# Performance work log

Measured on AMD Instinct MI355X. Metric: run time of the kernel, lower is better.

## Reference

```python
import jax, jax.numpy as jnp
import numpy as np

N = 100000      # nodes
E = 3200000     # edges (avg degree 32)
D = 128         # in_channels
H = 128         # hidden_channels
L = 4           # num_layers
G = 1000        # graphs in batch
C = 10          # out_channels
BN_EPS = 1e-5


def _init(key, shape, fan_in):
    return jax.random.normal(key, shape, jnp.float32) * jnp.float32(1.0 / np.sqrt(fan_in))


def setup_inputs() -> dict:
    key = jax.random.key(0)
    ks = jax.random.split(key, 12)
    x = jax.random.normal(ks[0], (N, D), jnp.float32)
    edge_index = jax.random.randint(ks[1], (2, E), 0, N)
    batch = jnp.sort(jax.random.randint(ks[2], (N,), 0, G))
    # stacked per-layer GINConv MLP params (in==hidden so all layers share shapes)
    W1 = _init(ks[3], (L, D, 2 * H), D)
    b1 = jnp.zeros((L, 2 * H), jnp.float32)
    g1 = jnp.ones((L, 2 * H), jnp.float32)
    bt1 = jnp.zeros((L, 2 * H), jnp.float32)
    W2 = _init(ks[4], (L, 2 * H, H), 2 * H)
    b2 = jnp.zeros((L, H), jnp.float32)
    g2 = jnp.ones((L, H), jnp.float32)
    bt2 = jnp.zeros((L, H), jnp.float32)
    eps = jnp.zeros((L,), jnp.float32)  # train_eps=True, init 0
    # final graph-level MLP
    Wm1 = _init(ks[5], (H, H), H)
    bm1 = jnp.zeros((H,), jnp.float32)
    gm = jnp.ones((H,), jnp.float32)
    btm = jnp.zeros((H,), jnp.float32)
    Wm2 = _init(ks[6], (H, C), H)
    bm2 = jnp.zeros((C,), jnp.float32)
    return dict(x=x, edge_index=edge_index, batch=batch, eps=eps,
                W1=W1, b1=b1, g1=g1, bt1=bt1, W2=W2, b2=b2, g2=g2, bt2=bt2,
                Wm1=Wm1, bm1=bm1, gm=gm, btm=btm, Wm2=Wm2, bm2=bm2)


def batchnorm(z, g, b):
    # training-mode BN: batch statistics, biased variance (torch semantics)
    m = jnp.mean(z, axis=0)
    v = jnp.mean(jnp.square(z - m), axis=0)
    return (z - m) * (g * jax.lax.rsqrt(v + BN_EPS)) + b


def reference(x, edge_index, batch, eps, W1, b1, g1, bt1, W2, b2, g2, bt2,
              Wm1, bm1, gm, btm, Wm2, bm2):
    src, dst = edge_index[0], edge_index[1]
    h = x
    for l in range(L):
        # GINConv: (1+eps)*x_i + sum_{j in N(i)} x_j, then MLP
        agg = jax.ops.segment_sum(h[src], dst, num_segments=N)  # [N, d]
        z = (1.0 + eps[l]) * h + agg
        z = jax.nn.relu(batchnorm(z @ W1[l] + b1[l], g1[l], bt1[l]))
        h = z @ W2[l] + b2[l]
        # outer per-layer BatchNorm + relu
        h = jax.nn.relu(batchnorm(h, g2[l], bt2[l]))
    # global_add_pool over graphs
    ge = jax.ops.segment_sum(h, batch, num_segments=G)  # [G, H]
    o = jax.nn.relu(batchnorm(ge @ Wm1 + bm1, gm, btm))  # dropout = identity (eval)
    return o @ Wm2 + bm2  # [G, C]
```

## Files before the change

### kernel.cpp

```cpp
#include <hip/hip_runtime.h>

#define N_NODES 100000
#define N_EDGES 3200000
#define NGRAPH  1000
#define NOUT    10
#define BN_EPS  1e-5f
#define CAP     96

#define SUM1 0
#define SQ1  256
#define S1   512
#define SH1  768
#define SUM2 1024
#define SQ2  1152
#define S2   1280
#define SH2  1408
#define SUMG 1536
#define SQG  1664
#define SG   1792
#define SHG  1920

typedef short v8s __attribute__((ext_vector_type(8)));
typedef float v4f __attribute__((ext_vector_type(4)));

__device__ __forceinline__ unsigned short f2bf(float x) {
    unsigned u = __float_as_uint(x);
    u += 0x7FFFu + ((u >> 16) & 1u);
    return (unsigned short)(u >> 16);
}
__device__ __forceinline__ float bf2f(unsigned short h) {
    return __uint_as_float(((unsigned)h) << 16);
}


__global__ void k_zero_i(int* p, int n) {
    int i = blockIdx.x * 256 + threadIdx.x;
    if (i < n) p[i] = 0;
}

__global__ void k_fillb(const int* __restrict__ ei, int* __restrict__ cnt,
                        int* __restrict__ csr) {
    const int lo = blockIdx.x * 12500;
    const int base = blockIdx.y * 2048 + threadIdx.x;
#pragma unroll
    for (int i = 0; i < 8; ++i) {
        int e = base + i * 256;
        if (e < N_EDGES) {
            int d = ei[N_EDGES + e];
            if ((unsigned)(d - lo) < 12500u) {
                int slot = atomicAdd(&cnt[d], 1);
                if (slot < CAP) csr[d * CAP + slot] = ei[e];
            }
        }
    }
}


__global__ void k_cvt0(const float* __restrict__ x, unsigned short* __restrict__ hb) {
    int i = blockIdx.x * 256 + threadIdx.x;
    float4 v = ((const float4*)x)[i];
    ushort4 o;
    o.x = f2bf(v.x); o.y = f2bf(v.y); o.z = f2bf(v.z); o.w = f2bf(v.w);
    ((ushort4*)hb)[i] = o;
}


__global__ void k_wsplit(const float* __restrict__ W1l, const float* __restrict__ W2l,
                         unsigned short* __restrict__ w1h, unsigned short* __restrict__ w1lo,
                         unsigned short* __restrict__ w2h, unsigned short* __restrict__ w2lo) {
    int idx = blockIdx.x * 256 + threadIdx.x;
    if (idx < 32768) {
        float v = W1l[idx];
        int k = idx >> 8, n = idx & 255;
        unsigned short h = f2bf(v);
        unsigned short l = f2bf(v - bf2f(h));
        int o = n * 128 + k;
        w1h[o] = h; w1lo[o] = l;
    } else {
        int i2 = idx - 32768;
        float v = W2l[i2];
        int k = i2 >> 7, n = i2 & 127;
        unsigned short h = f2bf(v);
        unsigned short l = f2bf(v - bf2f(h));
        int o = n * 256 + k;
        w2h[o] = h; w2lo[o] = l;
    }
}


template <bool BN>
__launch_bounds__(256)
__global__ void k_agg(const unsigned short* __restrict__ hb, unsigned short* __restrict__ zh,
                      unsigned short* __restrict__ zl, const int* __restrict__ cnt,
                      const int* __restrict__ csr, const float* __restrict__ eps, int l,
                      float* __restrict__ stats, const float* __restrict__ s,
                      const float* __restrict__ sh) {
    if (blockIdx.x == 0) {
        int t = threadIdx.x;
        stats[SUM1 + t] = 0.f;
        stats[SQ1 + t] = 0.f;
        if (t < 128) { stats[SUM2 + t] = 0.f; stats[SQ2 + t] = 0.f; }
    }
    int gtid = blockIdx.x * 256 + threadIdx.x;
    int node = gtid >> 6;
    int lane = gtid & 63;
    float2 sv = make_float2(1.f, 1.f), shv = make_float2(0.f, 0.f);
    if (BN) { sv = ((const float2*)s)[lane]; shv = ((const float2*)sh)[lane]; }
    float epv = 1.f + eps[l];
    const unsigned* h2 = (const unsigned*)hb;

    auto conv = [&](unsigned u) -> float2 {
        float a = bf2f((unsigned short)(u & 0xffffu));
        float b = bf2f((unsigned short)(u >> 16));
        if (BN) {
            a = fmaxf(fmaf(a, sv.x, shv.x), 0.f);
            b = fmaxf(fmaf(b, sv.y, shv.y), 0.f);
        }
        return make_float2(a, b);
    };

    float2 self = conv(h2[(size_t)node * 64 + lane]);
    float accx = epv * self.x, accy = epv * self.y;
    int d = min(cnt[node], CAP);
    const int* row = csr + node * CAP;
    int t = 0;
    for (; t + 1 < d; t += 2) {
        int j0 = row[t], j1 = row[t + 1];
        float2 v0 = conv(h2[(size_t)j0 * 64 + lane]);
        float2 v1 = conv(h2[(size_t)j1 * 64 + lane]);
        accx += v0.x + v1.x;
        accy += v0.y + v1.y;
    }
    if (t < d) {
        float2 v = conv(h2[(size_t)row[t] * 64 + lane]);
        accx += v.x;
        accy += v.y;
    }
    unsigned short hx = f2bf(accx), hy = f2bf(accy);
    unsigned short lx = f2bf(accx - bf2f(hx)), ly = f2bf(accy - bf2f(hy));
    ((unsigned*)zh)[(size_t)node * 64 + lane] = (unsigned)hx | ((unsigned)hy << 16);
    ((unsigned*)zl)[(size_t)node * 64 + lane] = (unsigned)lx | ((unsigned)ly << 16);
}


template <int K, int NC>
__launch_bounds__(256, 2)
__global__ void k_mgemm1(const unsigned short* __restrict__ Azh,
                         const unsigned short* __restrict__ Azl,
                         const unsigned short* __restrict__ Bhi,
                         const unsigned short* __restrict__ Blo,
                         const float* __restrict__ bias, float* __restrict__ Cm, int M,
                         float* __restrict__ osum, float* __restrict__ osq) {
    __shared__ unsigned short Ash[128 * 72];
    __shared__ unsigned short Asl[128 * 72];
    __shared__ unsigned short Bsh[128 * 72];
    __shared__ unsigned short Bsl[128 * 72];
    const int tid = threadIdx.x;
    const int lane = tid & 63;
    const int wid = tid >> 6;
    const int wm = wid >> 1, wn = wid & 1;
    const int lr = lane & 15;
    const int q = lane >> 4;
    const int r0 = blockIdx.x * 128;
    const int c0 = blockIdx.y * 128;

    v4f acc[16];
#pragma unroll
    for (int i = 0; i < 16; ++i) acc[i] = (v4f){0.f, 0.f, 0.f, 0.f};

    for (int kc = 0; kc < K; kc += 64) {
#pragma unroll
        for (int it = 0; it < 4; ++it) {
            int li = it * 256 + tid;
            int row = li >> 3, s8 = li & 7;
            int r = r0 + row;
            float4 vh = make_float4(0.f, 0.f, 0.f, 0.f);
            float4 vl = vh;
            if (r < M) {
                size_t go = (size_t)r * K + kc + s8 * 8;
                vh = *(const float4*)(Azh + go);
                vl = *(const float4*)(Azl + go);
            }
            int off = row * 72 + s8 * 8;
            *(float4*)&Ash[off] = vh;
            *(float4*)&Asl[off] = vl;
        }
#pragma unroll
        for (int it = 0; it < 4; ++it) {
            int li = it * 256 + tid;
            int n = li >> 3, s8 = li & 7;
            int off = n * 72 + s8 * 8;
            size_t go = (size_t)(c0 + n) * K + kc + s8 * 8;
            *(float4*)&Bsh[off] = *(const float4*)(Bhi + go);
            *(float4*)&Bsl[off] = *(const float4*)(Blo + go);
        }
        __syncthreads();
#pragma unroll
        for (int kk = 0; kk < 2; ++kk) {
            v8s ah[4], al[4], bh[4], bl[4];
#pragma unroll
            for (int t = 0; t < 4; ++t) {
                int aoff = (wm * 64 + t * 16 + lr) * 72 + kk * 32 + q * 8;
                ah[t] = *(const v8s*)&Ash[aoff];
                al[t] = *(const v8s*)&Asl[aoff];
                int boff = (wn * 64 + t * 16 + lr) * 72 + kk * 32 + q * 8;
                bh[t] = *(const v8s*)&Bsh[boff];
                bl[t] = *(const v8s*)&Bsl[boff];
            }
#pragma unroll
            for (int mt = 0; mt < 4; ++mt)
#pragma unroll
                for (int nt = 0; nt < 4; ++nt)
                    acc[mt * 4 + nt] = __builtin_amdgcn_mfma_f32_16x16x32_bf16(
                        ah[mt], bh[nt], acc[mt * 4 + nt], 0, 0, 0);
#pragma unroll
            for (int mt = 0; mt < 4; ++mt)
#pragma unroll
                for (int nt = 0; nt < 4; ++nt)
                    acc[mt * 4 + nt] = __builtin_amdgcn_mfma_f32_16x16x32_bf16(
                        ah[mt], bl[nt], acc[mt * 4 + nt], 0, 0, 0);
#pragma unroll
            for (int mt = 0; mt < 4; ++mt)
#pragma unroll
                for (int nt = 0; nt < 4; ++nt)
                    acc[mt * 4 + nt] = __builtin_amdgcn_mfma_f32_16x16x32_bf16(
                        al[mt], bh[nt], acc[mt * 4 + nt], 0, 0, 0);
        }
        __syncthreads();
    }

    float bias_v[4];
#pragma unroll
    for (int nt = 0; nt < 4; ++nt) bias_v[nt] = bias[c0 + wn * 64 + nt * 16 + lr];
    float ps[4] = {0.f, 0.f, 0.f, 0.f}, pq[4] = {0.f, 0.f, 0.f, 0.f};
#pragma unroll
    for (int mt = 0; mt < 4; ++mt) {
        int rb = r0 + wm * 64 + mt * 16 + q * 4;
#pragma unroll
        for (int r = 0; r < 4; ++r) {
            int row = rb + r;
            if (row < M) {
#pragma unroll
                for (int nt = 0; nt < 4; ++nt) {
                    float o = acc[mt * 4 + nt][r] + bias_v[nt];
                    Cm[(size_t)row * NC + c0 + wn * 64 + nt * 16 + lr] = o;
                    ps[nt] += o;
                    pq[nt] += o * o;
                }
            }
        }
    }
#pragma unroll
    for (int nt = 0; nt < 4; ++nt) {
        ps[nt] += __shfl_down(ps[nt], 16);
        ps[nt] += __shfl_down(ps[nt], 32);
        pq[nt] += __shfl_down(pq[nt], 16);
        pq[nt] += __shfl_down(pq[nt], 32);
    }
    if (lane < 16) {
#pragma unroll
        for (int nt = 0; nt < 4; ++nt) {
            int col = c0 + wn * 64 + nt * 16 + lane;
            atomicAdd(&osum[col], ps[nt]);
            atomicAdd(&osq[col], pq[nt]);
        }
    }
}


template <int K, int NC>
__launch_bounds__(256, 2)
__global__ void k_mgemm2(const float* __restrict__ A, const unsigned short* __restrict__ Bhi,
                         const unsigned short* __restrict__ Blo, const float* __restrict__ bias,
                         unsigned short* __restrict__ Cb, int M,
                         const float* __restrict__ ain_s, const float* __restrict__ ain_sh,
                         float* __restrict__ osum, float* __restrict__ osq) {
    __shared__ unsigned short Ash[128 * 72];
    __shared__ unsigned short Asl[128 * 72];
    __shared__ unsigned short Bsh[128 * 72];
    __shared__ unsigned short Bsl[128 * 72];
    const int tid = threadIdx.x;
    const int lane = tid & 63;
    const int wid = tid >> 6;
    const int wm = wid >> 1, wn = wid & 1;
    const int lr = lane & 15;
    const int q = lane >> 4;
    const int r0 = blockIdx.x * 128;
    const int c0 = blockIdx.y * 128;

    v4f acc[16];
#pragma unroll
    for (int i = 0; i < 16; ++i) acc[i] = (v4f){0.f, 0.f, 0.f, 0.f};

    for (int kc = 0; kc < K; kc += 64) {
#pragma unroll
        for (int it = 0; it < 8; ++it) {
            int li = it * 256 + tid;
            int row = li >> 4, s4 = li & 15;
            int r = r0 + row;
            float4 v = make_float4(0.f, 0.f, 0.f, 0.f);
            if (r < M) {
                v = *(const float4*)(A + (size_t)r * K + kc + s4 * 4);
                float4 s = *(const float4*)(ain_s + kc + s4 * 4);
                float4 h = *(const float4*)(ain_sh + kc + s4 * 4);
                v.x = fmaxf(fmaf(v.x, s.x, h.x), 0.f);
                v.y = fmaxf(fmaf(v.y, s.y, h.y), 0.f);
                v.z = fmaxf(fmaf(v.z, s.z, h.z), 0.f);
                v.w = fmaxf(fmaf(v.w, s.w, h.w), 0.f);
            }
            unsigned short h0 = f2bf(v.x), h1 = f2bf(v.y), h2 = f2bf(v.z), h3 = f2bf(v.w);
            unsigned short l0 = f2bf(v.x - bf2f(h0)), l1 = f2bf(v.y - bf2f(h1));
            unsigned short l2 = f2bf(v.z - bf2f(h2)), l3 = f2bf(v.w - bf2f(h3));
            int off = row * 72 + s4 * 4;
            *(short4*)&Ash[off] = make_short4((short)h0, (short)h1, (short)h2, (short)h3);
            *(short4*)&Asl[off] = make_short4((short)l0, (short)l1, (short)l2, (short)l3);
        }
#pragma unroll
        for (int it = 0; it < 4; ++it) {
            int li = it * 256 + tid;
            int n = li >> 3, s8 = li & 7;
            int off = n * 72 + s8 * 8;
            size_t go = (size_t)(c0 + n) * K + kc + s8 * 8;
            *(float4*)&Bsh[off] = *(const float4*)(Bhi + go);
            *(float4*)&Bsl[off] = *(const float4*)(Blo + go);
        }
        __syncthreads();
#pragma unroll
        for (int kk = 0; kk < 2; ++kk) {
            v8s ah[4], al[4], bh[4], bl[4];
#pragma unroll
            for (int t = 0; t < 4; ++t) {
                int aoff = (wm * 64 + t * 16 + lr) * 72 + kk * 32 + q * 8;
                ah[t] = *(const v8s*)&Ash[aoff];
                al[t] = *(const v8s*)&Asl[aoff];
                int boff = (wn * 64 + t * 16 + lr) * 72 + kk * 32 + q * 8;
                bh[t] = *(const v8s*)&Bsh[boff];
                bl[t] = *(const v8s*)&Bsl[boff];
            }
#pragma unroll
            for (int mt = 0; mt < 4; ++mt)
#pragma unroll
                for (int nt = 0; nt < 4; ++nt)
                    acc[mt * 4 + nt] = __builtin_amdgcn_mfma_f32_16x16x32_bf16(
                        ah[mt], bh[nt], acc[mt * 4 + nt], 0, 0, 0);
#pragma unroll
            for (int mt = 0; mt < 4; ++mt)
#pragma unroll
                for (int nt = 0; nt < 4; ++nt)
                    acc[mt * 4 + nt] = __builtin_amdgcn_mfma_f32_16x16x32_bf16(
                        ah[mt], bl[nt], acc[mt * 4 + nt], 0, 0, 0);
#pragma unroll
            for (int mt = 0; mt < 4; ++mt)
#pragma unroll
                for (int nt = 0; nt < 4; ++nt)
                    acc[mt * 4 + nt] = __builtin_amdgcn_mfma_f32_16x16x32_bf16(
                        al[mt], bh[nt], acc[mt * 4 + nt], 0, 0, 0);
        }
        __syncthreads();
    }

    float bias_v[4];
#pragma unroll
    for (int nt = 0; nt < 4; ++nt) bias_v[nt] = bias[c0 + wn * 64 + nt * 16 + lr];
    float ps[4] = {0.f, 0.f, 0.f, 0.f}, pq[4] = {0.f, 0.f, 0.f, 0.f};
#pragma unroll
    for (int mt = 0; mt < 4; ++mt) {
        int rb = r0 + wm * 64 + mt * 16 + q * 4;
#pragma unroll
        for (int r = 0; r < 4; ++r) {
            int row = rb + r;
            if (row < M) {
#pragma unroll
                for (int nt = 0; nt < 4; ++nt) {
                    float o = acc[mt * 4 + nt][r] + bias_v[nt];
                    Cb[(size_t)row * NC + c0 + wn * 64 + nt * 16 + lr] = f2bf(o);
                    ps[nt] += o;
                    pq[nt] += o * o;
                }
            }
        }
    }
#pragma unroll
    for (int nt = 0; nt < 4; ++nt) {
        ps[nt] += __shfl_down(ps[nt], 16);
        ps[nt] += __shfl_down(ps[nt], 32);
        pq[nt] += __shfl_down(pq[nt], 16);
        pq[nt] += __shfl_down(pq[nt], 32);
    }
    if (lane < 16) {
#pragma unroll
        for (int nt = 0; nt < 4; ++nt) {
            int col = c0 + wn * 64 + nt * 16 + lane;
            atomicAdd(&osum[col], ps[nt]);
            atomicAdd(&osq[col], pq[nt]);
        }
    }
}


template <int K, int NC, bool AIN, bool STATS>
__launch_bounds__(256)
__global__ void k_gemm(const float* __restrict__ A, const float* __restrict__ Bg,
                       const float* __restrict__ bias, float* __restrict__ Cm, int M,
                       const float* __restrict__ ain_s, const float* __restrict__ ain_sh,
                       float* __restrict__ osum, float* __restrict__ osq) {
    __shared__ __align__(16) float As[64][68];
    __shared__ __align__(16) float Bs[64][68];
    const int tid = threadIdx.x;
    const int tx = tid & 15, ty = tid >> 4;
    const int r0 = blockIdx.x * 64;
    const int c0 = blockIdx.y * 64;
    float acc[4][4] = {};

    for (int kc = 0; kc < K; kc += 64) {
#pragma unroll
        for (int it = 0; it < 4; ++it) {
            int li = it * 256 + tid;
            int row = li >> 4, f4 = li & 15;
            int r = r0 + row;
            float4 v = make_float4(0.f, 0.f, 0.f, 0.f);
            if (r < M) v = *(const float4*)(A + (size_t)r * K + kc + f4 * 4);
            As[f4 * 4 + 0][row] = v.x;
            As[f4 * 4 + 1][row] = v.y;
            As[f4 * 4 + 2][row] = v.z;
            As[f4 * 4 + 3][row] = v.w;
        }
#pragma unroll
        for (int it = 0; it < 4; ++it) {
            int li = it * 256 + tid;
            int krow = li >> 4, f4 = li & 15;
            float4 v = *(const float4*)(Bg + (size_t)(kc + krow) * NC + c0 + f4 * 4);
            *(float4*)&Bs[krow][f4 * 4] = v;
        }
        __syncthreads();
#pragma unroll
        for (int k = 0; k < 64; ++k) {
            float4 a = *(const float4*)&As[k][ty * 4];
            float4 b = *(const float4*)&Bs[k][tx * 4];
            float av[4] = {a.x, a.y, a.z, a.w};
            float bv[4] = {b.x, b.y, b.z, b.w};
#pragma unroll
            for (int i = 0; i < 4; ++i)
#pragma unroll
                for (int j = 0; j < 4; ++j) acc[i][j] = fmaf(av[i], bv[j], acc[i][j]);
        }
        __syncthreads();
    }

    const int c = c0 + tx * 4;
    float4 bb = *(const float4*)(bias + c);
    float bvv[4] = {bb.x, bb.y, bb.z, bb.w};
    float ps[4] = {0.f, 0.f, 0.f, 0.f};
    float pq[4] = {0.f, 0.f, 0.f, 0.f};
#pragma unroll
    for (int i = 0; i < 4; ++i) {
        int r = r0 + ty * 4 + i;
        if (r < M) {
            float o[4];
#pragma unroll
            for (int j = 0; j < 4; ++j) {
                o[j] = acc[i][j] + bvv[j];
                if (STATS) { ps[j] += o[j]; pq[j] += o[j] * o[j]; }
            }
            float4 ov = make_float4(o[0], o[1], o[2], o[3]);
            *(float4*)(Cm + (size_t)r * NC + c) = ov;
        }
    }
    if (STATS) {
        float* rs = &As[0][0];
        float* rq = &Bs[0][0];
        *(float4*)&rs[ty * 68 + tx * 4] = make_float4(ps[0], ps[1], ps[2], ps[3]);
        *(float4*)&rq[ty * 68 + tx * 4] = make_float4(pq[0], pq[1], pq[2], pq[3]);
        __syncthreads();
        if (tid < 16) {
#pragma unroll
            for (int j = 0; j < 4; ++j) {
                float s = 0.f, q = 0.f;
                for (int t = 0; t < 16; ++t) {
                    s += rs[t * 68 + tid * 4 + j];
                    q += rq[t * 68 + tid * 4 + j];
                }
                atomicAdd(&osum[c0 + tid * 4 + j], s);
                atomicAdd(&osq[c0 + tid * 4 + j], q);
            }
        }
    }
}


__global__ void k_bnstats(const float* __restrict__ sum, const float* __restrict__ sq,
                          const float* __restrict__ g, const float* __restrict__ bt,
                          float* __restrict__ s, float* __restrict__ sh, int n, float invM) {
    int i = threadIdx.x;
    if (i < n) {
        float m = sum[i] * invM;
        float v = sq[i] * invM - m * m;
        float sc = g[i] * rsqrtf(v + BN_EPS);
        s[i] = sc;
        sh[i] = bt[i] - m * sc;
    }
}


__global__ void k_zero2_f(float* p1, int n1, float* p2, int n2) {
    int i = blockIdx.x * 256 + threadIdx.x;
    if (i < n1) p1[i] = 0.f;
    else if (i - n1 < n2) p2[i - n1] = 0.f;
}

__global__ void k_pool(const unsigned short* __restrict__ hb, const int* __restrict__ batch,
                       float* __restrict__ ge, const float* __restrict__ s,
                       const float* __restrict__ sh) {
    int t = blockIdx.x * 256 + threadIdx.x;
    int node = t >> 6, lane = t & 63;
    int g = batch[node];
    unsigned u = ((const unsigned*)hb)[(size_t)node * 64 + lane];
    float2 sv = ((const float2*)s)[lane];
    float2 shv = ((const float2*)sh)[lane];
    float a = fmaxf(fmaf(bf2f((unsigned short)(u & 0xffffu)), sv.x, shv.x), 0.f);
    float b = fmaxf(fmaf(bf2f((unsigned short)(u >> 16)), sv.y, shv.y), 0.f);
    float* p = ge + (size_t)g * 128 + lane * 2;
    atomicAdd(p, a);
    atomicAdd(p + 1, b);
}


__global__ void k_final(const float* __restrict__ gmid, const float* __restrict__ sg,
                        const float* __restrict__ shg, const float* __restrict__ Wm2,
                        const float* __restrict__ bm2, float* __restrict__ out) {
    int idx = blockIdx.x * 256 + threadIdx.x;
    if (idx >= NGRAPH * NOUT) return;
    int g = idx / NOUT, c = idx % NOUT;
    const float* row = gmid + (size_t)g * 128;
    float acc = bm2[c];
#pragma unroll 8
    for (int k = 0; k < 128; ++k) {
        float y = fmaxf(fmaf(row[k], sg[k], shg[k]), 0.f);
        acc = fmaf(y, Wm2[k * NOUT + c], acc);
    }
    out[idx] = acc;
}


extern "C" void kernel_launch(void* const* d_in, const int* in_sizes, int n_in,
                              void* d_out, int out_size, void* d_ws, size_t ws_size,
                              hipStream_t stream) {
    const float* x   = (const float*)d_in[0];
    const int*   ei  = (const int*)d_in[1];
    const int* batch = (const int*)d_in[2];
    const float* eps = (const float*)d_in[3];
    const float* W1  = (const float*)d_in[4];
    const float* b1  = (const float*)d_in[5];
    const float* g1  = (const float*)d_in[6];
    const float* bt1 = (const float*)d_in[7];
    const float* W2  = (const float*)d_in[8];
    const float* b2  = (const float*)d_in[9];
    const float* g2  = (const float*)d_in[10];
    const float* bt2 = (const float*)d_in[11];
    const float* Wm1 = (const float*)d_in[12];
    const float* bm1 = (const float*)d_in[13];
    const float* gm  = (const float*)d_in[14];
    const float* btm = (const float*)d_in[15];
    const float* Wm2 = (const float*)d_in[16];
    const float* bm2 = (const float*)d_in[17];
    float* out = (float*)d_out;

    float* W = (float*)d_ws;
    float* bufC  = W;
    float* stats = W + 25600000;
    float* ge    = W + 25602048;
    float* gmid  = W + 25730048;
    int* ib      = (int*)(W + 25858048);
    int* cnt = ib;
    int* csr = ib + 100000;
    unsigned short* wt = (unsigned short*)(ib + 9700000);
    unsigned short* w1h = wt;
    unsigned short* w1l = wt + 32768;
    unsigned short* w2h = wt + 65536;
    unsigned short* w2l = wt + 98304;
    unsigned short* hb = wt + 131072;
    unsigned short* zh = hb + 12800000;
    unsigned short* zl = zh + 12800000;

    k_zero_i<<<391, 256, 0, stream>>>(cnt, N_NODES);
    k_fillb<<<dim3(8, 1563), 256, 0, stream>>>(ei, cnt, csr);
    k_cvt0<<<12500, 256, 0, stream>>>(x, hb);

    for (int l = 0; l < 4; ++l) {
        k_wsplit<<<256, 256, 0, stream>>>(W1 + l * 32768, W2 + l * 32768,
                                          w1h, w1l, w2h, w2l);
        if (l == 0)
            k_agg<false><<<25000, 256, 0, stream>>>(hb, zh, zl, cnt, csr, eps, l, stats,
                                                    nullptr, nullptr);
        else
            k_agg<true><<<25000, 256, 0, stream>>>(hb, zh, zl, cnt, csr, eps, l, stats,
                                                   stats + S2, stats + SH2);
        k_mgemm1<128, 256><<<dim3(782, 2), 256, 0, stream>>>(
            zh, zl, w1h, w1l, b1 + l * 256, bufC, N_NODES, stats + SUM1, stats + SQ1);
        k_bnstats<<<1, 256, 0, stream>>>(stats + SUM1, stats + SQ1, g1 + l * 256,
                                         bt1 + l * 256, stats + S1, stats + SH1, 256,
                                         1.f / N_NODES);
        k_mgemm2<256, 128><<<dim3(782, 1), 256, 0, stream>>>(
            bufC, w2h, w2l, b2 + l * 128, hb, N_NODES,
            stats + S1, stats + SH1, stats + SUM2, stats + SQ2);
        k_bnstats<<<1, 128, 0, stream>>>(stats + SUM2, stats + SQ2, g2 + l * 128,
                                         bt2 + l * 128, stats + S2, stats + SH2, 128,
                                         1.f / N_NODES);
    }

    k_zero2_f<<<502, 256, 0, stream>>>(ge, 128000, stats + SUMG, 256);
    k_pool<<<25000, 256, 0, stream>>>(hb, batch, ge, stats + S2, stats + SH2);
    k_gemm<128, 128, false, true><<<dim3(16, 2), 256, 0, stream>>>(
        ge, Wm1, bm1, gmid, NGRAPH, nullptr, nullptr, stats + SUMG, stats + SQG);
    k_bnstats<<<1, 128, 0, stream>>>(stats + SUMG, stats + SQG, gm, btm,
                                     stats + SG, stats + SHG, 128, 1.f / NGRAPH);
    k_final<<<40, 256, 0, stream>>>(gmid, stats + SG, stats + SHG, Wm2, bm2, out);
}
```

Before: 1.782 ms.

## Precompute BN+ReLU activations once and widen aggregation gathers to 16-byte loads

Adds a k_bnapply pass that applies the previous layer's BN scale/shift and ReLU to every node once, writing a bf16 copy. Aggregation can then gather already-normalised rows instead of redoing the affine and ReLU for each of the ~32 edges per node. The gather kernel now assigns 16 lanes per node with uint4 loads (8 bf16 channels per lane) and reads neighbour indices as int4, so each load instruction moves more data. Pooling is also reworked so each thread sums 8 consecutive nodes and flushes atomics only when the graph id changes, cutting atomic traffic. The cost is an extra full read and write of the activation buffer per layer and a larger workspace.

```diff
diff --git a/kernel.cpp b/kernel.cpp
--- a/kernel.cpp
+++ b/kernel.cpp
@@ -62,6 +62,31 @@
     ushort4 o;
     o.x = f2bf(v.x); o.y = f2bf(v.y); o.z = f2bf(v.z); o.w = f2bf(v.w);
     ((ushort4*)hb)[i] = o;
+}
+
+
+__global__ void k_bnapply(const unsigned short* __restrict__ hb,
+                          unsigned short* __restrict__ yb,
+                          const float* __restrict__ s, const float* __restrict__ sh) {
+    int i = blockIdx.x * 256 + threadIdx.x;
+    int c16 = i & 15;
+    uint4 u = ((const uint4*)hb)[i];
+    float4 sA = ((const float4*)s)[c16 * 2], sB = ((const float4*)s)[c16 * 2 + 1];
+    float4 hA = ((const float4*)sh)[c16 * 2], hB = ((const float4*)sh)[c16 * 2 + 1];
+    float y0 = fmaxf(fmaf(__uint_as_float(u.x << 16),        sA.x, hA.x), 0.f);
+    float y1 = fmaxf(fmaf(__uint_as_float(u.x & 0xffff0000u), sA.y, hA.y), 0.f);
+    float y2 = fmaxf(fmaf(__uint_as_float(u.y << 16),        sA.z, hA.z), 0.f);
+    float y3 = fmaxf(fmaf(__uint_as_float(u.y & 0xffff0000u), sA.w, hA.w), 0.f);
+    float y4 = fmaxf(fmaf(__uint_as_float(u.z << 16),        sB.x, hB.x), 0.f);
+    float y5 = fmaxf(fmaf(__uint_as_float(u.z & 0xffff0000u), sB.y, hB.y), 0.f);
+    float y6 = fmaxf(fmaf(__uint_as_float(u.w << 16),        sB.z, hB.z), 0.f);
+    float y7 = fmaxf(fmaf(__uint_as_float(u.w & 0xffff0000u), sB.w, hB.w), 0.f);
+    uint4 o;
+    o.x = (unsigned)f2bf(y0) | ((unsigned)f2bf(y1) << 16);
+    o.y = (unsigned)f2bf(y2) | ((unsigned)f2bf(y3) << 16);
+    o.z = (unsigned)f2bf(y4) | ((unsigned)f2bf(y5) << 16);
+    o.w = (unsigned)f2bf(y6) | ((unsigned)f2bf(y7) << 16);
+    ((uint4*)yb)[i] = o;
 }
 
 
@@ -88,58 +113,103 @@
 }
 
 
-template <bool BN>
 __launch_bounds__(256)
-__global__ void k_agg(const unsigned short* __restrict__ hb, unsigned short* __restrict__ zh,
+__global__ void k_agg(const unsigned short* __restrict__ yb, unsigned short* __restrict__ zh,
                       unsigned short* __restrict__ zl, const int* __restrict__ cnt,
                       const int* __restrict__ csr, const float* __restrict__ eps, int l,
-                      float* __restrict__ stats, const float* __restrict__ s,
-                      const float* __restrict__ sh) {
+                      float* __restrict__ stats) {
     if (blockIdx.x == 0) {
         int t = threadIdx.x;
         stats[SUM1 + t] = 0.f;
         stats[SQ1 + t] = 0.f;
         if (t < 128) { stats[SUM2 + t] = 0.f; stats[SQ2 + t] = 0.f; }
     }
-    int gtid = blockIdx.x * 256 + threadIdx.x;
-    int node = gtid >> 6;
-    int lane = gtid & 63;
-    float2 sv = make_float2(1.f, 1.f), shv = make_float2(0.f, 0.f);
-    if (BN) { sv = ((const float2*)s)[lane]; shv = ((const float2*)sh)[lane]; }
+    const int tid = threadIdx.x;
+    const int wid = tid >> 6, lane = tid & 63;
+    const int q = lane >> 4, sl = lane & 15;
+    const int node = blockIdx.x * 16 + wid * 4 + q;
+    const uint4* y4 = (const uint4*)yb;
+    const size_t selfo = (size_t)node * 16 + sl;
+
     float epv = 1.f + eps[l];
-    const unsigned* h2 = (const unsigned*)hb;
-
-    auto conv = [&](unsigned u) -> float2 {
-        float a = bf2f((unsigned short)(u & 0xffffu));
-        float b = bf2f((unsigned short)(u >> 16));
-        if (BN) {
-            a = fmaxf(fmaf(a, sv.x, shv.x), 0.f);
-            b = fmaxf(fmaf(b, sv.y, shv.y), 0.f);
-        }
-        return make_float2(a, b);
-    };
-
-    float2 self = conv(h2[(size_t)node * 64 + lane]);
-    float accx = epv * self.x, accy = epv * self.y;
+    uint4 su = y4[selfo];
+    float acc[8];
+    acc[0] = epv * __uint_as_float(su.x << 16);
+    acc[1] = epv * __uint_as_float(su.x & 0xffff0000u);
+    acc[2] = epv * __uint_as_float(su.y << 16);
+    acc[3] = epv * __uint_as_float(su.y & 0xffff0000u);
+    acc[4] = epv * __uint_as_float(su.z << 16);
+    acc[5] = epv * __uint_as_float(su.z & 0xffff0000u);
+    acc[6] = epv * __uint_as_float(su.w << 16);
+    acc[7] = epv * __uint_as_float(su.w & 0xffff0000u);
+
     int d = min(cnt[node], CAP);
     const int* row = csr + node * CAP;
     int t = 0;
-    for (; t + 1 < d; t += 2) {
-        int j0 = row[t], j1 = row[t + 1];
-        float2 v0 = conv(h2[(size_t)j0 * 64 + lane]);
-        float2 v1 = conv(h2[(size_t)j1 * 64 + lane]);
-        accx += v0.x + v1.x;
-        accy += v0.y + v1.y;
-    }
-    if (t < d) {
-        float2 v = conv(h2[(size_t)row[t] * 64 + lane]);
-        accx += v.x;
-        accy += v.y;
-    }
-    unsigned short hx = f2bf(accx), hy = f2bf(accy);
-    unsigned short lx = f2bf(accx - bf2f(hx)), ly = f2bf(accy - bf2f(hy));
-    ((unsigned*)zh)[(size_t)node * 64 + lane] = (unsigned)hx | ((unsigned)hy << 16);
-    ((unsigned*)zl)[(size_t)node * 64 + lane] = (unsigned)lx | ((unsigned)ly << 16);
+    for (; t + 3 < d; t += 4) {
+        int4 jv = *(const int4*)(row + t);
+        uint4 v0 = y4[(size_t)jv.x * 16 + sl];
+        uint4 v1 = y4[(size_t)jv.y * 16 + sl];
+        uint4 v2 = y4[(size_t)jv.z * 16 + sl];
+        uint4 v3 = y4[(size_t)jv.w * 16 + sl];
+        acc[0] += __uint_as_float(v0.x << 16);
+        acc[1] += __uint_as_float(v0.x & 0xffff0000u);
+        acc[2] += __uint_as_float(v0.y << 16);
+        acc[3] += __uint_as_float(v0.y & 0xffff0000u);
+        acc[4] += __uint_as_float(v0.z << 16);
+        acc[5] += __uint_as_float(v0.z & 0xffff0000u);
+        acc[6] += __uint_as_float(v0.w << 16);
+        acc[7] += __uint_as_float(v0.w & 0xffff0000u);
+        acc[0] += __uint_as_float(v1.x << 16);
+        acc[1] += __uint_as_float(v1.x & 0xffff0000u);
+        acc[2] += __uint_as_float(v1.y << 16);
+        acc[3] += __uint_as_float(v1.y & 0xffff0000u);
+        acc[4] += __uint_as_float(v1.z << 16);
+        acc[5] += __uint_as_float(v1.z & 0xffff0000u);
+        acc[6] += __uint_as_float(v1.w << 16);
+        acc[7] += __uint_as_float(v1.w & 0xffff0000u);
+        acc[0] += __uint_as_float(v2.x << 16);
+        acc[1] += __uint_as_float(v2.x & 0xffff0000u);
+        acc[2] += __uint_as_float(v2.y << 16);
+        acc[3] += __uint_as_float(v2.y & 0xffff0000u);
+        acc[4] += __uint_as_float(v2.z << 16);
+        acc[5] += __uint_as_float(v2.z & 0xffff0000u);
+        acc[6] += __uint_as_float(v2.w << 16);
+        acc[7] += __uint_as_float(v2.w & 0xffff0000u);
+        acc[0] += __uint_as_float(v3.x << 16);
+        acc[1] += __uint_as_float(v3.x & 0xffff0000u);
+        acc[2] += __uint_as_float(v3.y << 16);
+        acc[3] += __uint_as_float(v3.y & 0xffff0000u);
+        acc[4] += __uint_as_float(v3.z << 16);
+        acc[5] += __uint_as_float(v3.z & 0xffff0000u);
+        acc[6] += __uint_as_float(v3.w << 16);
+        acc[7] += __uint_as_float(v3.w & 0xffff0000u);
+    }
+    for (; t < d; ++t) {
+        uint4 v = y4[(size_t)row[t] * 16 + sl];
+        acc[0] += __uint_as_float(v.x << 16);
+        acc[1] += __uint_as_float(v.x & 0xffff0000u);
+        acc[2] += __uint_as_float(v.y << 16);
+        acc[3] += __uint_as_float(v.y & 0xffff0000u);
+        acc[4] += __uint_as_float(v.z << 16);
+        acc[5] += __uint_as_float(v.z & 0xffff0000u);
+        acc[6] += __uint_as_float(v.w << 16);
+        acc[7] += __uint_as_float(v.w & 0xffff0000u);
+    }
+
+    unsigned oh[4], ol[4];
+#pragma unroll
+    for (int w = 0; w < 4; ++w) {
+        float a = acc[2 * w], b = acc[2 * w + 1];
+        unsigned short ha = f2bf(a), hb_ = f2bf(b);
+        unsigned short la = f2bf(a - bf2f(ha)), lb = f2bf(b - bf2f(hb_));
+        oh[w] = (unsigned)ha | ((unsigned)hb_ << 16);
+        ol[w] = (unsigned)la | ((unsigned)lb << 16);
+    }
+    uint4 vh; vh.x = oh[0]; vh.y = oh[1]; vh.z = oh[2]; vh.w = oh[3];
+    uint4 vl; vl.x = ol[0]; vl.y = ol[1]; vl.z = ol[2]; vl.w = ol[3];
+    ((uint4*)zh)[selfo] = vh;
+    ((uint4*)zl)[selfo] = vl;
 }
 
 
@@ -512,16 +582,30 @@
                        float* __restrict__ ge, const float* __restrict__ s,
                        const float* __restrict__ sh) {
     int t = blockIdx.x * 256 + threadIdx.x;
-    int node = t >> 6, lane = t & 63;
-    int g = batch[node];
-    unsigned u = ((const unsigned*)hb)[(size_t)node * 64 + lane];
-    float2 sv = ((const float2*)s)[lane];
-    float2 shv = ((const float2*)sh)[lane];
-    float a = fmaxf(fmaf(bf2f((unsigned short)(u & 0xffffu)), sv.x, shv.x), 0.f);
-    float b = fmaxf(fmaf(bf2f((unsigned short)(u >> 16)), sv.y, shv.y), 0.f);
-    float* p = ge + (size_t)g * 128 + lane * 2;
-    atomicAdd(p, a);
-    atomicAdd(p + 1, b);
+    int c = t & 63;
+    int n0 = (t >> 6) * 8;
+    float2 sv = ((const float2*)s)[c];
+    float2 shv = ((const float2*)sh)[c];
+    const unsigned* h2 = (const unsigned*)hb;
+    float ax = 0.f, ay = 0.f;
+    int gcur = batch[n0];
+#pragma unroll
+    for (int k = 0; k < 8; ++k) {
+        int n = n0 + k;
+        int g = batch[n];
+        if (g != gcur) {
+            float* p = ge + (size_t)gcur * 128 + c * 2;
+            atomicAdd(p, ax);
+            atomicAdd(p + 1, ay);
+            ax = 0.f; ay = 0.f; gcur = g;
+        }
+        unsigned u = h2[(size_t)n * 64 + c];
+        ax += fmaxf(fmaf(__uint_as_float(u << 16), sv.x, shv.x), 0.f);
+        ay += fmaxf(fmaf(__uint_as_float(u & 0xffff0000u), sv.y, shv.y), 0.f);
+    }
+    float* p = ge + (size_t)gcur * 128 + c * 2;
+    atomicAdd(p, ax);
+    atomicAdd(p + 1, ay);
 }
 
 
@@ -581,6 +665,7 @@
     unsigned short* hb = wt + 131072;
     unsigned short* zh = hb + 12800000;
     unsigned short* zl = zh + 12800000;
+    unsigned short* yb = zl + 12800000;
 
     k_zero_i<<<391, 256, 0, stream>>>(cnt, N_NODES);
     k_fillb<<<dim3(8, 1563), 256, 0, stream>>>(ei, cnt, csr);
@@ -589,12 +674,14 @@
     for (int l = 0; l < 4; ++l) {
         k_wsplit<<<256, 256, 0, stream>>>(W1 + l * 32768, W2 + l * 32768,
                                           w1h, w1l, w2h, w2l);
-        if (l == 0)
-            k_agg<false><<<25000, 256, 0, stream>>>(hb, zh, zl, cnt, csr, eps, l, stats,
-                                                    nullptr, nullptr);
-        else
-            k_agg<true><<<25000, 256, 0, stream>>>(hb, zh, zl, cnt, csr, eps, l, stats,
-                                                   stats + S2, stats + SH2);
+        const unsigned short* ysrc;
+        if (l == 0) {
+            ysrc = hb;
+        } else {
+            k_bnapply<<<6250, 256, 0, stream>>>(hb, yb, stats + S2, stats + SH2);
+            ysrc = yb;
+        }
+        k_agg<<<6250, 256, 0, stream>>>(ysrc, zh, zl, cnt, csr, eps, l, stats);
         k_mgemm1<128, 256><<<dim3(782, 2), 256, 0, stream>>>(
             zh, zl, w1h, w1l, b1 + l * 256, bufC, N_NODES, stats + SUM1, stats + SQ1);
         k_bnstats<<<1, 256, 0, stream>>>(stats + SUM1, stats + SQ1, g1 + l * 256,
@@ -609,7 +696,7 @@
     }
 
     k_zero2_f<<<502, 256, 0, stream>>>(ge, 128000, stats + SUMG, 256);
-    k_pool<<<25000, 256, 0, stream>>>(hb, batch, ge, stats + S2, stats + SH2);
+    k_pool<<<3125, 256, 0, stream>>>(hb, batch, ge, stats + S2, stats + SH2);
     k_gemm<128, 128, false, true><<<dim3(16, 2), 256, 0, stream>>>(
         ge, Wm1, bm1, gmid, NGRAPH, nullptr, nullptr, stats + SUMG, stats + SQG);
     k_bnstats<<<1, 128, 0, stream>>>(stats + SUMG, stats + SQG, gm, btm,
```

New measurement: 1.513 ms. -15.1%, faster.
